# Kernel optimization log

Hardware: AMD Instinct MI355X
Metric: run time of the kernel (lower is better)

The kernel has to match this reference:

```python
import jax, jax.numpy as jnp
import numpy as np

B = 524288
IN_DIM = 16
OUT_DIM = 32  # hidden_dim3
N_CHUNKS = 4
CHUNK = 4


def ste_round(x):
    # straight-through round (grad passes unchanged, like Round.apply)
    return x + jax.lax.stop_gradient(jnp.round(x) - x)


def ste_sign(x):
    # straight-through sign (grad passes unchanged, like Sign.apply)
    return x + jax.lax.stop_gradient(jnp.sign(x) - x)


def setup_inputs() -> dict:
    key = jax.random.key(0)
    k1, k2 = jax.random.split(key)
    Input = jax.random.uniform(k1, (B, IN_DIM), dtype=jnp.float32)
    weight = jax.random.normal(k2, (OUT_DIM, IN_DIM), dtype=jnp.float32)
    InMin = jnp.float32(0.0)
    InMax = jnp.float32(1.0)
    return {"Input": Input, "weight": weight, "InMin": InMin, "InMax": InMax}


def reference(Input, weight, InMin, InMax):
    # eval-mode forward of QuantLinear
    scale = InMax - InMin
    w = ste_sign(weight)                       # [O, I] in {-1, 0, 1}
    wP = jax.nn.relu(w)                        # positive mask
    wM = jax.nn.relu(-w)                       # negative mask

    # 4-bit input quantization (eval path): clip(round((x-min)/(max-min)*15), 0, 15)
    q = jnp.clip(ste_round((Input - InMin) / scale * 15.0), 0.0, 15.0)  # [B, I]

    # bias = linear(InMin * ones, w): each row = InMin * sum_j w[o, j]
    bias = InMin * jnp.sum(w, axis=1)          # [O], broadcasts over batch

    # chunked 4-wide linears, vectorized over the 4 chunks
    qc = q.reshape(B, N_CHUNKS, CHUNK)         # [B, C, 4]
    wPc = wP.reshape(OUT_DIM, N_CHUNKS, CHUNK)  # [O, C, 4]
    wMc = wM.reshape(OUT_DIM, N_CHUNKS, CHUNK)
    yP = jnp.einsum('bcf,ocf->cbo', qc, wPc)   # [C, B, O]
    yM = jnp.einsum('bcf,ocf->cbo', qc, wMc)   # [C, B, O]

    # accumulate clip(round(y/15), -4, 4) * (InMax - InMin) over all 8 terms
    terms = jnp.clip(ste_round(yP / 15.0), -4.0, 4.0) \
          + jnp.clip(ste_round(-yM / 15.0), -4.0, 4.0)  # [C, B, O]
    x = jnp.sum(terms, axis=0) * scale + bias  # [B, O]
    return x
```

## Files before the change

kernel.cpp:

```cpp
#include <hip/hip_runtime.h>
#include <stdint.h>


#if __has_builtin(__builtin_amdgcn_sdot4)
#define HAVE_SDOT4 1
#else
#define HAVE_SDOT4 0
#endif

typedef float f32x4 __attribute__((ext_vector_type(4)));

__device__ __forceinline__ int dot7(uint32_t q, uint32_t m) {
#if HAVE_SDOT4
    return __builtin_amdgcn_sdot4((int)q, (int)m, 7, false);
#else
    return (int)(((q & m) * 0x01010101u) >> 24) + 7;
#endif
}

__device__ __forceinline__ int r15(int y7) {
    return (int)(((uint32_t)y7 * 274u) >> 12);
}

__global__ void qlin_prep(const float* __restrict__ wgt,
                          const float* __restrict__ pmin,
                          uint32_t* __restrict__ ws)
{
    const int t = threadIdx.x;
    const uint32_t MASKBYTE = HAVE_SDOT4 ? 1u : 0xFFu;
    {
        int o = t >> 3, k = t & 7, c = k & 3, isM = k >> 2;
        const float* wrow = wgt + o * 16 + c * 4;
        uint32_t m = 0;
#pragma unroll
        for (int j = 0; j < 4; ++j) {
            float v = wrow[j];
            bool sel = isM ? (v < 0.0f) : (v > 0.0f);
            if (sel) m |= MASKBYTE << (8 * j);
        }
        ws[o * 8 + isM * 4 + c] = m;
    }
    if (t < 32) {
        const float* wrow = wgt + t * 16;
        int s = 0;
#pragma unroll
        for (int j = 0; j < 16; ++j) {
            float v = wrow[j];
            s += (v > 0.0f) ? 1 : 0;
            s -= (v < 0.0f) ? 1 : 0;
        }
        ((float*)ws)[256 + t] = __fmul_rn(pmin[0], (float)s);
    }
}

__global__ __launch_bounds__(256) void qlin_main(
    const float* __restrict__ in, const uint32_t* __restrict__ ws,
    const float* __restrict__ pmin, const float* __restrict__ pmax,
    float* __restrict__ out, int nrows)
{
    __shared__ __align__(16) uint32_t xpose[256];
    const int t = threadIdx.x;
    const int lane = t & 63;
    const int wv = t >> 6;
    const size_t R0 = ((size_t)blockIdx.x * 4 + wv) * 64;
    (void)nrows;

    const float4* inp = (const float4*)in + R0 * 4 + lane;
    float4 fa = inp[0];
    float4 fb = inp[64];

    const int ogrp = lane & 7;
    const int rsel = lane >> 3;
    uint32_t* xp = xpose + (wv << 6);

    const uint4* mw = (const uint4*)ws;
    const uint4 MP0 = mw[(ogrp * 4 + 0) * 2], MM0 = mw[(ogrp * 4 + 0) * 2 + 1];
    const uint4 MP1 = mw[(ogrp * 4 + 1) * 2], MM1 = mw[(ogrp * 4 + 1) * 2 + 1];
    const uint4 MP2 = mw[(ogrp * 4 + 2) * 2], MM2 = mw[(ogrp * 4 + 2) * 2 + 1];
    const uint4 MP3 = mw[(ogrp * 4 + 3) * 2], MM3 = mw[(ogrp * 4 + 3) * 2 + 1];
    const float4 bias = ((const float4*)((const float*)ws + 256))[ogrp];

    const float InMin = pmin[0];
    const float scale = __fsub_rn(pmax[0], InMin);
    const bool unit = (scale == 1.0f);

#define QUANT(F, QW)                                                        \
    {                                                                       \
        float e[4] = { F.x, F.y, F.z, F.w };                                \
        uint32_t pk = 0;                                                    \
        _Pragma("unroll")                                                   \
        for (int j = 0; j < 4; ++j) {                                       \
            float d  = __fsub_rn(e[j], InMin);                              \
            float sd;                                                       \
            if (unit) sd = d; else sd = __fdiv_rn(d, scale);                \
            float v  = __fmul_rn(sd, 15.0f);                                \
            float rr = rintf(v);                                            \
            rr = fminf(fmaxf(rr, 0.0f), 15.0f);                             \
            pk |= ((uint32_t)(int)rr) << (8 * j);                           \
        }                                                                   \
        QW = pk;                                                            \
    }

#define ROWCOMP(q0, q1, q2, q3, dst)                                        \
        {                                                                   \
            int a0 = r15(dot7(q0, MP0.x)) - r15(dot7(q0, MM0.x))            \
                   + r15(dot7(q1, MP0.y)) - r15(dot7(q1, MM0.y))            \
                   + r15(dot7(q2, MP0.z)) - r15(dot7(q2, MM0.z))            \
                   + r15(dot7(q3, MP0.w)) - r15(dot7(q3, MM0.w));           \
            int a1 = r15(dot7(q0, MP1.x)) - r15(dot7(q0, MM1.x))            \
                   + r15(dot7(q1, MP1.y)) - r15(dot7(q1, MM1.y))            \
                   + r15(dot7(q2, MP1.z)) - r15(dot7(q2, MM1.z))            \
                   + r15(dot7(q3, MP1.w)) - r15(dot7(q3, MM1.w));           \
            int a2 = r15(dot7(q0, MP2.x)) - r15(dot7(q0, MM2.x))            \
                   + r15(dot7(q1, MP2.y)) - r15(dot7(q1, MM2.y))            \
                   + r15(dot7(q2, MP2.z)) - r15(dot7(q2, MM2.z))            \
                   + r15(dot7(q3, MP2.w)) - r15(dot7(q3, MM2.w));           \
            int a3 = r15(dot7(q0, MP3.x)) - r15(dot7(q0, MM3.x))            \
                   + r15(dot7(q1, MP3.y)) - r15(dot7(q1, MM3.y))            \
                   + r15(dot7(q2, MP3.z)) - r15(dot7(q2, MM3.z))            \
                   + r15(dot7(q3, MP3.w)) - r15(dot7(q3, MM3.w));           \
            f32x4 res;                                                      \
            res.x = __fadd_rn(__fmul_rn((float)a0, scale), bias.x);         \
            res.y = __fadd_rn(__fmul_rn((float)a1, scale), bias.y);         \
            res.z = __fadd_rn(__fmul_rn((float)a2, scale), bias.z);         \
            res.w = __fadd_rn(__fmul_rn((float)a3, scale), bias.w);         \
            __builtin_nontemporal_store(res, (f32x4*)(dst));                \
        }

#define SLAB(F, K, PRELOAD)                                                 \
    {                                                                       \
        uint32_t qw;                                                        \
        QUANT(F, qw);                                                       \
        xp[lane] = qw;                                                      \
        PRELOAD                                                             \
        const uint4 qA = *(const uint4*)(xp + (rsel << 2));                 \
        const uint4 qB = *(const uint4*)(xp + 32 + (rsel << 2));            \
        float* p0 = out + (R0 + (size_t)(K) * 16 + rsel) * 32 + (ogrp << 2);\
        ROWCOMP(qA.x, qA.y, qA.z, qA.w, p0);                                \
        ROWCOMP(qB.x, qB.y, qB.z, qB.w, p0 + 256);                          \
    }

    SLAB(fa, 0, fa = inp[128];)
    SLAB(fb, 1, fb = inp[192];)
    SLAB(fa, 2, )
    SLAB(fb, 3, )

#undef SLAB
#undef ROWCOMP
#undef QUANT
}

extern "C" void kernel_launch(void* const* d_in, const int* in_sizes, int n_in,
                              void* d_out, int out_size, void* d_ws, size_t ws_size,
                              hipStream_t stream) {
    (void)n_in; (void)ws_size; (void)out_size;
    const float* in  = (const float*)d_in[0];
    const float* wgt = (const float*)d_in[1];
    const float* mn  = (const float*)d_in[2];
    const float* mx  = (const float*)d_in[3];
    float* out = (float*)d_out;
    uint32_t* ws = (uint32_t*)d_ws;
    const int nrows = in_sizes[0] / 16;
    const int blocks = nrows / 256;

    qlin_prep<<<1, 256, 0, stream>>>(wgt, mn, ws);
    qlin_main<<<blocks, 256, 0, stream>>>(in, ws, mn, mx, out, nrows);
}
```

Measured before the change: 106.8 us.

## Fuse weight prep into main kernel and use udot4 plus LDS rounding LUT

Removes the separate weight-prep kernel launch: each block now builds sign masks and bias in shared memory from the raw weights, plus an 8.7KB int8 lookup table of r15(p)-r15(m). The positive and negative halves are packed into one udot4 per chunk (weights 1 and 128), and the LUT turns each result into the combined rounded term, halving dot ops and removing the multiply-shift rounding. All four input float4 loads are issued up front. The cost is that every block redoes the weight prep and LUT fill, syncs once, and pays LDS lookups in the inner loop.

```diff
diff --git a/kernel.cpp b/kernel.cpp
--- a/kernel.cpp
+++ b/kernel.cpp
@@ -2,43 +2,62 @@
 #include <stdint.h>
 
 
-#if __has_builtin(__builtin_amdgcn_sdot4)
-#define HAVE_SDOT4 1
+#if __has_builtin(__builtin_amdgcn_udot4)
+#define HAVE_UDOT4 1
 #else
-#define HAVE_SDOT4 0
+#define HAVE_UDOT4 0
 #endif
 
 typedef float f32x4 __attribute__((ext_vector_type(4)));
 
-__device__ __forceinline__ int dot7(uint32_t q, uint32_t m) {
-#if HAVE_SDOT4
-    return __builtin_amdgcn_sdot4((int)q, (int)m, 7, false);
+__device__ __forceinline__ int r15i(int x) { return (x * 274) >> 12; }
+
+__global__ __launch_bounds__(256) void qlin_main(
+    const float* __restrict__ in, const float* __restrict__ wgt,
+    const float* __restrict__ pmin, const float* __restrict__ pmax,
+    float* __restrict__ out, int nrows)
+{
+    __shared__ int8_t lut[8704];
+#if HAVE_UDOT4
+    __shared__ __align__(16) uint32_t cmask[128];
 #else
-    return (int)(((q & m) * 0x01010101u) >> 24) + 7;
+    __shared__ __align__(16) uint32_t cmaskP[128];
+    __shared__ __align__(16) uint32_t cmaskM[128];
 #endif
-}
+    __shared__ __align__(16) float sbias[32];
+    __shared__ __align__(16) uint32_t xpose[256];
 
-__device__ __forceinline__ int r15(int y7) {
-    return (int)(((uint32_t)y7 * 274u) >> 12);
-}
+    const int t = threadIdx.x;
+    const int lane = t & 63;
+    const int wv = t >> 6;
+    const size_t R0 = ((size_t)blockIdx.x * 4 + wv) * 64;
+    (void)nrows;
 
-__global__ void qlin_prep(const float* __restrict__ wgt,
-                          const float* __restrict__ pmin,
-                          uint32_t* __restrict__ ws)
-{
-    const int t = threadIdx.x;
-    const uint32_t MASKBYTE = HAVE_SDOT4 ? 1u : 0xFFu;
-    {
-        int o = t >> 3, k = t & 7, c = k & 3, isM = k >> 2;
+    const float4* inp = (const float4*)in + R0 * 4 + lane;
+    float4 f0 = inp[0], f1 = inp[64], f2 = inp[128], f3 = inp[192];
+
+    if (t < 128) {
+        const int o = t >> 2, c = t & 3;
         const float* wrow = wgt + o * 16 + c * 4;
+#if HAVE_UDOT4
         uint32_t m = 0;
 #pragma unroll
         for (int j = 0; j < 4; ++j) {
             float v = wrow[j];
-            bool sel = isM ? (v < 0.0f) : (v > 0.0f);
-            if (sel) m |= MASKBYTE << (8 * j);
+            if (v > 0.0f)      m |= 1u   << (8 * j);
+            else if (v < 0.0f) m |= 128u << (8 * j);
         }
-        ws[o * 8 + isM * 4 + c] = m;
+        cmask[t] = m;
+#else
+        uint32_t mp = 0, mm = 0;
+#pragma unroll
+        for (int j = 0; j < 4; ++j) {
+            float v = wrow[j];
+            if (v > 0.0f) mp |= 0xFFu << (8 * j);
+            if (v < 0.0f) mm |= 0xFFu << (8 * j);
+        }
+        cmaskP[t] = mp; cmaskM[t] = mm;
+#endif
     }
     if (t < 32) {
         const float* wrow = wgt + t * 16;
@@ -49,36 +68,36 @@
             s += (v > 0.0f) ? 1 : 0;
             s -= (v < 0.0f) ? 1 : 0;
         }
-        ((float*)ws)[256 + t] = __fmul_rn(pmin[0], (float)s);
+        sbias[t] = __fmul_rn(pmin[0], (float)s);
     }
-}
-
-__global__ __launch_bounds__(256) void qlin_main(
-    const float* __restrict__ in, const uint32_t* __restrict__ ws,
-    const float* __restrict__ pmin, const float* __restrict__ pmax,
-    float* __restrict__ out, int nrows)
-{
-    __shared__ __align__(16) uint32_t xpose[256];
-    const int t = threadIdx.x;
-    const int lane = t & 63;
-    const int wv = t >> 6;
-    const size_t R0 = ((size_t)blockIdx.x * 4 + wv) * 64;
-    (void)nrows;
-
-    const float4* inp = (const float4*)in + R0 * 4 + lane;
-    float4 fa = inp[0];
-    float4 fb = inp[64];
+    for (int i = t; i < 8704; i += 256)
+        lut[i] = (int8_t)(r15i(i & 127) - r15i(i >> 7));
+    __syncthreads();
 
     const int ogrp = lane & 7;
     const int rsel = lane >> 3;
     uint32_t* xp = xpose + (wv << 6);
 
-    const uint4* mw = (const uint4*)ws;
-    const uint4 MP0 = mw[(ogrp * 4 + 0) * 2], MM0 = mw[(ogrp * 4 + 0) * 2 + 1];
-    const uint4 MP1 = mw[(ogrp * 4 + 1) * 2], MM1 = mw[(ogrp * 4 + 1) * 2 + 1];
-    const uint4 MP2 = mw[(ogrp * 4 + 2) * 2], MM2 = mw[(ogrp * 4 + 2) * 2 + 1];
-    const uint4 MP3 = mw[(ogrp * 4 + 3) * 2], MM3 = mw[(ogrp * 4 + 3) * 2 + 1];
-    const float4 bias = ((const float4*)((const float*)ws + 256))[ogrp];
+#if HAVE_UDOT4
+    const uint4 cm0 = *(const uint4*)&cmask[(ogrp * 4 + 0) * 4];
+    const uint4 cm1 = *(const uint4*)&cmask[(ogrp * 4 + 1) * 4];
+    const uint4 cm2 = *(const uint4*)&cmask[(ogrp * 4 + 2) * 4];
+    const uint4 cm3 = *(const uint4*)&cmask[(ogrp * 4 + 3) * 4];
+#define TERM(q, m) ((int)lut[(int)__builtin_amdgcn_udot4((q), (m), 903u, false)])
+#else
+    const uint4 cp0 = *(const uint4*)&cmaskP[(ogrp * 4 + 0) * 4];
+    const uint4 cp1 = *(const uint4*)&cmaskP[(ogrp * 4 + 1) * 4];
+    const uint4 cp2 = *(const uint4*)&cmaskP[(ogrp * 4 + 2) * 4];
+    const uint4 cp3 = *(const uint4*)&cmaskP[(ogrp * 4 + 3) * 4];
+    const uint4 cn0 = *(const uint4*)&cmaskM[(ogrp * 4 + 0) * 4];
+    const uint4 cn1 = *(const uint4*)&cmaskM[(ogrp * 4 + 1) * 4];
+    const uint4 cn2 = *(const uint4*)&cmaskM[(ogrp * 4 + 2) * 4];
+    const uint4 cn3 = *(const uint4*)&cmaskM[(ogrp * 4 + 3) * 4];
+#define TERM2(q, mp, mm)                                                     \
+    ((int)lut[(int)((((q) & (mp)) * 0x01010101u) >> 24)                      \
+            + ((int)((((q) & (mm)) * 0x01010101u) >> 24) << 7) + 903])
+#endif
+    const float4 bias = *(const float4*)(sbias + ogrp * 4);
 
     const float InMin = pmin[0];
     const float scale = __fsub_rn(pmax[0], InMin);
@@ -101,24 +120,15 @@
         QW = pk;                                                            \
     }
 
+#if HAVE_UDOT4
+#define ACC4(q0, q1, q2, q3, cm) \
+    (TERM(q0, cm.x) + TERM(q1, cm.y) + TERM(q2, cm.z) + TERM(q3, cm.w))
 #define ROWCOMP(q0, q1, q2, q3, dst)                                        \
         {                                                                   \
-            int a0 = r15(dot7(q0, MP0.x)) - r15(dot7(q0, MM0.x))            \
-                   + r15(dot7(q1, MP0.y)) - r15(dot7(q1, MM0.y))            \
-                   + r15(dot7(q2, MP0.z)) - r15(dot7(q2, MM0.z))            \
-                   + r15(dot7(q3, MP0.w)) - r15(dot7(q3, MM0.w));           \
-            int a1 = r15(dot7(q0, MP1.x)) - r15(dot7(q0, MM1.x))            \
-                   + r15(dot7(q1, MP1.y)) - r15(dot7(q1, MM1.y))            \
-                   + r15(dot7(q2, MP1.z)) - r15(dot7(q2, MM1.z))            \
-                   + r15(dot7(q3, MP1.w)) - r15(dot7(q3, MM1.w));           \
-            int a2 = r15(dot7(q0, MP2.x)) - r15(dot7(q0, MM2.x))            \
-                   + r15(dot7(q1, MP2.y)) - r15(dot7(q1, MM2.y))            \
-                   + r15(dot7(q2, MP2.z)) - r15(dot7(q2, MM2.z))            \
-                   + r15(dot7(q3, MP2.w)) - r15(dot7(q3, MM2.w));           \
-            int a3 = r15(dot7(q0, MP3.x)) - r15(dot7(q0, MM3.x))            \
-                   + r15(dot7(q1, MP3.y)) - r15(dot7(q1, MM3.y))            \
-                   + r15(dot7(q2, MP3.z)) - r15(dot7(q2, MM3.z))            \
-                   + r15(dot7(q3, MP3.w)) - r15(dot7(q3, MM3.w));           \
+            int a0 = ACC4(q0, q1, q2, q3, cm0);                             \
+            int a1 = ACC4(q0, q1, q2, q3, cm1);                             \
+            int a2 = ACC4(q0, q1, q2, q3, cm2);                             \
+            int a3 = ACC4(q0, q1, q2, q3, cm3);                             \
             f32x4 res;                                                      \
             res.x = __fadd_rn(__fmul_rn((float)a0, scale), bias.x);         \
             res.y = __fadd_rn(__fmul_rn((float)a1, scale), bias.y);         \
@@ -126,13 +136,30 @@
             res.w = __fadd_rn(__fmul_rn((float)a3, scale), bias.w);         \
             __builtin_nontemporal_store(res, (f32x4*)(dst));                \
         }
+#else
+#define ACC4F(q0, q1, q2, q3, cp, cn)                                       \
+    (TERM2(q0, cp.x, cn.x) + TERM2(q1, cp.y, cn.y) +                        \
+     TERM2(q2, cp.z, cn.z) + TERM2(q3, cp.w, cn.w))
+#define ROWCOMP(q0, q1, q2, q3, dst)                                        \
+        {                                                                   \
+            int a0 = ACC4F(q0, q1, q2, q3, cp0, cn0);                       \
+            int a1 = ACC4F(q0, q1, q2, q3, cp1, cn1);                       \
+            int a2 = ACC4F(q0, q1, q2, q3, cp2, cn2);                       \
+            int a3 = ACC4F(q0, q1, q2, q3, cp3, cn3);                       \
+            f32x4 res;                                                      \
+            res.x = __fadd_rn(__fmul_rn((float)a0, scale), bias.x);         \
+            res.y = __fadd_rn(__fmul_rn((float)a1, scale), bias.y);         \
+            res.z = __fadd_rn(__fmul_rn((float)a2, scale), bias.z);         \
+            res.w = __fadd_rn(__fmul_rn((float)a3, scale), bias.w);         \
+            __builtin_nontemporal_store(res, (f32x4*)(dst));                \
+        }
+#endif
 
-#define SLAB(F, K, PRELOAD)                                                 \
+#define SLAB(F, K)                                                          \
     {                                                                       \
         uint32_t qw;                                                        \
         QUANT(F, qw);                                                       \
         xp[lane] = qw;                                                      \
-        PRELOAD                                                             \
         const uint4 qA = *(const uint4*)(xp + (rsel << 2));                 \
         const uint4 qB = *(const uint4*)(xp + 32 + (rsel << 2));            \
         float* p0 = out + (R0 + (size_t)(K) * 16 + rsel) * 32 + (ogrp << 2);\
@@ -140,10 +167,10 @@
         ROWCOMP(qB.x, qB.y, qB.z, qB.w, p0 + 256);                          \
     }
 
-    SLAB(fa, 0, fa = inp[128];)
-    SLAB(fb, 1, fb = inp[192];)
-    SLAB(fa, 2, )
-    SLAB(fb, 3, )
+    SLAB(f0, 0)
+    SLAB(f1, 1)
+    SLAB(f2, 2)
+    SLAB(f3, 3)
 
 #undef SLAB
 #undef ROWCOMP
@@ -153,16 +180,13 @@
 extern "C" void kernel_launch(void* const* d_in, const int* in_sizes, int n_in,
                               void* d_out, int out_size, void* d_ws, size_t ws_size,
                               hipStream_t stream) {
-    (void)n_in; (void)ws_size; (void)out_size;
+    (void)n_in; (void)d_ws; (void)ws_size; (void)out_size;
     const float* in  = (const float*)d_in[0];
     const float* wgt = (const float*)d_in[1];
     const float* mn  = (const float*)d_in[2];
     const float* mx  = (const float*)d_in[3];
     float* out = (float*)d_out;
-    uint32_t* ws = (uint32_t*)d_ws;
     const int nrows = in_sizes[0] / 16;
     const int blocks = nrows / 256;
-
-    qlin_prep<<<1, 256, 0, stream>>>(wgt, mn, ws);
-    qlin_main<<<blocks, 256, 0, stream>>>(in, ws, mn, mx, out, nrows);
+    qlin_main<<<blocks, 256, 0, stream>>>(in, wgt, mn, mx, out, nrows);
 }
```

New measurement: 106.9 us. Within noise of the previous version (+0.1%).
